# Kernel optimization log

Measured on AMD Instinct MI355X. Metric: run time of the kernel, lower is better.

## Reference

```python
import jax, jax.numpy as jnp
import numpy as np

HIDDEN = 16
PROJ = 2
INPUT = 2


def _gates_split(gates):
    # PyTorch LSTM gate order: input, forget, cell(g), output
    i, f, g, o = jnp.split(gates, 4, axis=-1)
    return jax.nn.sigmoid(i), jax.nn.sigmoid(f), jnp.tanh(g), jax.nn.sigmoid(o)


def setup_inputs() -> dict:
    key = jax.random.key(0)
    ks = jax.random.split(key, 7)
    B, T, nstep = 64, 8192, 4096
    bound = 1.0 / np.sqrt(HIDDEN)  # torch default LSTM init: U(-1/sqrt(H), 1/sqrt(H))
    u = lambda k, shp: jax.random.uniform(k, shp, jnp.float32, -bound, bound)
    return {
        "u_train": jax.random.normal(ks[0], (B, T, INPUT), jnp.float32),
        "y_train": jax.random.normal(ks[1], (B, T, INPUT), jnp.float32),
        "W_ih": u(ks[2], (4 * HIDDEN, INPUT)),   # weight_ih_l0
        "W_hh": u(ks[3], (4 * HIDDEN, PROJ)),    # weight_hh_l0 (proj_size -> input to gates)
        "b_ih": u(ks[4], (4 * HIDDEN,)),
        "b_hh": u(ks[5], (4 * HIDDEN,)),
        "W_hr": u(ks[6], (PROJ, HIDDEN)),        # projection weight_hr_l0
        "nstep": nstep,
    }


def reference(u_train, y_train, W_ih, W_hh, b_ih, b_hh, W_hr, nstep):
    b = b_ih + b_hh

    # --- estimate_state: each of the nstep single-step LSTM calls starts from
    # ZERO state (the original never threads state back in), so there is no
    # recurrence: vectorize over all nstep timesteps at once.
    x = y_train[:, :nstep, :]                       # [B, nstep, 2]
    gates = jnp.einsum("bti,gi->btg", x, W_ih) + b  # [B, nstep, 4H]; h-term is 0
    i, f, g, o = _gates_split(gates)
    c1 = i * g                                      # c0 = 0 => f*c0 vanishes
    y1 = jnp.einsum("bth,ph->btp", o * jnp.tanh(c1), W_hr)  # [B, nstep, PROJ]
    hn = y1[:, -1, :]                               # [B, PROJ]
    cn = c1[:, -1, :]                               # [B, HIDDEN]

    # --- predict_state: true recurrent LSTM with projection over the tail.
    def step(carry, x_t):
        h, c = carry                                # h:[B,PROJ] c:[B,HIDDEN]
        gt = x_t @ W_ih.T + h @ W_hh.T + b          # [B, 4H]
        i, f, g, o = _gates_split(gt)
        c = f * c + i * g
        h = (o * jnp.tanh(c)) @ W_hr.T              # [B, PROJ]
        return (h, c), h

    xs = jnp.swapaxes(u_train[:, nstep:, :], 0, 1)  # [T-nstep, B, 2]
    _, ys = jax.lax.scan(step, (hn, cn), xs)
    y2 = jnp.swapaxes(ys, 0, 1)                     # [B, T-nstep, PROJ]

    return jnp.concatenate([y1, y2], axis=1)        # [B, T, PROJ]
```

## Files before the change

kernel.cpp:

```cpp
#include <hip/hip_runtime.h>


#define BB   64
#define TT   8192
#define NST  4096
#define PF   16

static __device__ __forceinline__ float fast_exp2(float x) {
#if __has_builtin(__builtin_amdgcn_exp2f)
  return __builtin_amdgcn_exp2f(x);
#else
  return exp2f(x);
#endif
}
static __device__ __forceinline__ float fast_rcp(float x) {
#if __has_builtin(__builtin_amdgcn_rcpf)
  return __builtin_amdgcn_rcpf(x);
#else
  return 1.0f / x;
#endif
}

template <int CTRL>
static __device__ __forceinline__ float rr_add(float x) {
  int r = __builtin_amdgcn_update_dpp(0, __builtin_bit_cast(int, x), CTRL, 0xF, 0xF, true);
  return x + __builtin_bit_cast(float, r);
}

template <int SEL>
static __device__ __forceinline__ float qperm(float x) {
  int r = __builtin_amdgcn_update_dpp(0, __builtin_bit_cast(int, x), SEL, 0xF, 0xF, true);
  return __builtin_bit_cast(float, r);
}

static __device__ __forceinline__ float rdlane63(float x) {
  return __builtin_bit_cast(float,
      __builtin_amdgcn_readlane(__builtin_bit_cast(int, x), 63));
}

struct SW {
  float w0, w1, wh0, wh1, b;
  float m, n;
  float whr0, whr0m2, whr1, whr1m2;
};

static __device__ __forceinline__ void scan_step(const SW& w, float x0, float x1,
                                                 float& h0, float& h1, float& c) {
  const float bse = fmaf(w.w1, x1, fmaf(w.w0, x0, w.b));
  float s = fmaf(w.wh0, h0, bse);
  s = fmaf(w.wh1, h1, s);
  const float d = fast_rcp(1.f + fast_exp2(s));
  const float a = fmaf(d, w.m, w.n);
  const float gi = qperm<0x00>(a);
  const float gf = qperm<0x55>(a);
  const float gg = qperm<0xAA>(a);
  const float go = qperm<0xFF>(a);
  c = fmaf(gf, c, gi * gg);
  const float o0  = go * w.whr0;
  const float o0m = go * w.whr0m2;
  const float o1  = go * w.whr1;
  const float o1m = go * w.whr1m2;
  const float r2 = fast_rcp(1.f + fast_exp2(c * 2.8853900817779268f));
  float p0 = fmaf(r2, o0m, o0);
  float p1 = fmaf(r2, o1m, o1);
  p0 = rr_add<0x124>(p0); p1 = rr_add<0x124>(p1);
  p0 = rr_add<0x128>(p0); p1 = rr_add<0x128>(p1);
  p0 = rr_add<0x142>(p0); p1 = rr_add<0x142>(p1);
  p0 = rr_add<0x143>(p0); p1 = rr_add<0x143>(p1);
  h0 = rdlane63(p0);
  h1 = rdlane63(p1);
}

__global__ __launch_bounds__(256) void openlstm_kernel(
    const float* __restrict__ u_train, const float* __restrict__ y_train,
    const float* __restrict__ Wih, const float* __restrict__ Whh,
    const float* __restrict__ bih, const float* __restrict__ bhh,
    const float* __restrict__ Whr, float* __restrict__ out) {
  const int tid = threadIdx.x;
  const float S1 = -1.4426950408889634f;
  const float S2 = -2.8853900817779268f;

  if (blockIdx.x < 16) {
    const int lane = tid & 63;
    const int wv   = tid >> 6;
    const int bb   = blockIdx.x * 4 + wv;
    const int hh   = lane >> 2;
    const int r    = lane & 3;
    const int wrow = r * 16 + hh;
    const bool isg = (r == 2);
    const float sc = isg ? S2 : S1;

    SW w;
    w.w0  = Wih[2 * wrow] * sc;  w.w1  = Wih[2 * wrow + 1] * sc;
    w.wh0 = Whh[2 * wrow] * sc;  w.wh1 = Whh[2 * wrow + 1] * sc;
    w.b   = (bih[wrow] + bhh[wrow]) * sc;
    w.m   = isg ? 2.f : 1.f;
    w.n   = isg ? -1.f : 0.f;
    w.whr0   = Whr[hh];
    w.whr0m2 = -2.f * w.whr0;
    w.whr1   = Whr[16 + hh];
    w.whr1m2 = -2.f * w.whr1;

    float h0 = 0.f, h1 = 0.f, c = 0.f;
    {
      const float2 xv = *(const float2*)(y_train + ((size_t)bb * TT + (NST - 1)) * 2);
      scan_step(w, xv.x, xv.y, h0, h1, c);
    }

    const float* up = u_train + ((size_t)bb * TT + NST) * 2;
    float*       ob = out     + ((size_t)bb * TT + NST) * 2;

    float2 xb[PF];
#pragma unroll
    for (int k = 0; k < PF; ++k) xb[k] = *(const float2*)(up + 2 * k);

    const int  cslot = lane >> 1;
    const bool odd   = lane & 1;
    float cap = 0.f;

    for (int t = 0; t < NST; t += PF) {
#pragma unroll
      for (int k = 0; k < PF; ++k) {
        const float x0 = xb[k].x, x1 = xb[k].y;
        int tn = t + k + PF;
        tn = (tn < NST) ? tn : (NST - 1);
        xb[k] = *(const float2*)(up + (size_t)tn * 2);
        scan_step(w, x0, x1, h0, h1, c);
        const float hsel = odd ? h1 : h0;
        cap = (cslot == k) ? hsel : cap;
      }
      if (lane < 32) ob[(size_t)t * 2 + lane] = cap;
    }
  } else {
    const int hh  = tid & 15;
    const int grp = tid >> 4;
    const int gid = (blockIdx.x - 16) * 16 + grp;
    const int bb  = gid >> 12;
    const int t   = gid & (NST - 1);
    const int ri = hh, rg = hh + 32, ro = hh + 48;

    const float wii0 = Wih[2 * ri] * S1, wii1 = Wih[2 * ri + 1] * S1;
    const float wig0 = Wih[2 * rg] * S2, wig1 = Wih[2 * rg + 1] * S2;
    const float wio0 = Wih[2 * ro] * S1, wio1 = Wih[2 * ro + 1] * S1;
    const float bi = (bih[ri] + bhh[ri]) * S1;
    const float bg = (bih[rg] + bhh[rg]) * S2;
    const float bo = (bih[ro] + bhh[ro]) * S1;
    const float whr0 = Whr[hh], whr1 = Whr[16 + hh];

    const float2 xv = *(const float2*)(y_train + ((size_t)bb * TT + t) * 2);
    const float si = fmaf(wii1, xv.y, fmaf(wii0, xv.x, bi));
    const float sg = fmaf(wig1, xv.y, fmaf(wig0, xv.x, bg));
    const float so = fmaf(wio1, xv.y, fmaf(wio0, xv.x, bo));
    const float gi = fast_rcp(1.f + fast_exp2(si));
    const float gg = fmaf(2.f, fast_rcp(1.f + fast_exp2(sg)), -1.f);
    const float go = fast_rcp(1.f + fast_exp2(so));
    const float c1 = gi * gg;
    const float tc = fmaf(-2.f, fast_rcp(1.f + fast_exp2(c1 * 2.8853900817779268f)), 1.f);
    const float v  = go * tc;
    float p0 = v * whr0;
    float p1 = v * whr1;
    p0 = rr_add<0x128>(p0); p1 = rr_add<0x128>(p1);
    p0 = rr_add<0x124>(p0); p1 = rr_add<0x124>(p1);
    p0 = rr_add<0x122>(p0); p1 = rr_add<0x122>(p1);
    p0 = rr_add<0x121>(p0); p1 = rr_add<0x121>(p1);
    if (hh == 0) *(float2*)(out + ((size_t)bb * TT + t) * 2) = make_float2(p0, p1);
  }
}

extern "C" void kernel_launch(void* const* d_in, const int* in_sizes, int n_in,
                              void* d_out, int out_size, void* d_ws, size_t ws_size,
                              hipStream_t stream) {
  const float* u_train = (const float*)d_in[0];
  const float* y_train = (const float*)d_in[1];
  const float* Wih     = (const float*)d_in[2];
  const float* Whh     = (const float*)d_in[3];
  const float* bih     = (const float*)d_in[4];
  const float* bhh     = (const float*)d_in[5];
  const float* Whr     = (const float*)d_in[6];
  float* out = (float*)d_out;

  const int grid = 16 + (BB * NST) / 16;
  openlstm_kernel<<<grid, 256, 0, stream>>>(u_train, y_train, Wih, Whh, bih,
                                            bhh, Whr, out);
}
```

Before: 457.8 us.

## Prescale cell state, raise scan wave priority, simplify input prefetch and output stores

The recurrent cell state is now kept prescaled by 2*log2(e), with the g-gate affine constants adjusted to match, so one multiply drops off the serial critical path each step. The scan waves call s_setprio(1) so they get scheduling priority over the co-resident parallel-phase waves. The 16-deep register prefetch ring and lane-captured 32-wide stores are replaced by a one-step-ahead float4 load covering two timesteps and a per-pair float4 store from every lane. The shallower prefetch could expose load latency on the serial chain, and having every lane store each pair adds redundant memory traffic.

```diff
diff --git a/kernel.cpp b/kernel.cpp
--- a/kernel.cpp
+++ b/kernel.cpp
@@ -4,7 +4,6 @@
 #define BB   64
 #define TT   8192
 #define NST  4096
-#define PF   16
 
 static __device__ __forceinline__ float fast_exp2(float x) {
 #if __has_builtin(__builtin_amdgcn_exp2f)
@@ -45,7 +44,7 @@
 };
 
 static __device__ __forceinline__ void scan_step(const SW& w, float x0, float x1,
-                                                 float& h0, float& h1, float& c) {
+                                                 float& h0, float& h1, float& C) {
   const float bse = fmaf(w.w1, x1, fmaf(w.w0, x0, w.b));
   float s = fmaf(w.wh0, h0, bse);
   s = fmaf(w.wh1, h1, s);
@@ -55,12 +54,12 @@
   const float gf = qperm<0x55>(a);
   const float gg = qperm<0xAA>(a);
   const float go = qperm<0xFF>(a);
-  c = fmaf(gf, c, gi * gg);
+  C = fmaf(gf, C, gi * gg);
   const float o0  = go * w.whr0;
   const float o0m = go * w.whr0m2;
   const float o1  = go * w.whr1;
   const float o1m = go * w.whr1m2;
-  const float r2 = fast_rcp(1.f + fast_exp2(c * 2.8853900817779268f));
+  const float r2 = fast_rcp(1.f + fast_exp2(C));
   float p0 = fmaf(r2, o0m, o0);
   float p1 = fmaf(r2, o1m, o1);
   p0 = rr_add<0x124>(p0); p1 = rr_add<0x124>(p1);
@@ -81,6 +80,7 @@
   const float S2 = -2.8853900817779268f;
 
   if (blockIdx.x < 16) {
+    __builtin_amdgcn_s_setprio(1);
     const int lane = tid & 63;
     const int wv   = tid >> 6;
     const int bb   = blockIdx.x * 4 + wv;
@@ -94,42 +94,37 @@
     w.w0  = Wih[2 * wrow] * sc;  w.w1  = Wih[2 * wrow + 1] * sc;
     w.wh0 = Whh[2 * wrow] * sc;  w.wh1 = Whh[2 * wrow + 1] * sc;
     w.b   = (bih[wrow] + bhh[wrow]) * sc;
-    w.m   = isg ? 2.f : 1.f;
-    w.n   = isg ? -1.f : 0.f;
+    w.m   = isg ? 5.7707801635558536f : 1.f;
+    w.n   = isg ? -2.8853900817779268f : 0.f;
     w.whr0   = Whr[hh];
     w.whr0m2 = -2.f * w.whr0;
     w.whr1   = Whr[16 + hh];
     w.whr1m2 = -2.f * w.whr1;
 
-    float h0 = 0.f, h1 = 0.f, c = 0.f;
+    float h0 = 0.f, h1 = 0.f, C = 0.f;
     {
       const float2 xv = *(const float2*)(y_train + ((size_t)bb * TT + (NST - 1)) * 2);
-      scan_step(w, xv.x, xv.y, h0, h1, c);
+      scan_step(w, xv.x, xv.y, h0, h1, C);
     }
 
     const float* up = u_train + ((size_t)bb * TT + NST) * 2;
-    float*       ob = out     + ((size_t)bb * TT + NST) * 2;
+    float*       op = out     + ((size_t)bb * TT + NST) * 2;
 
-    float2 xb[PF];
-#pragma unroll
-    for (int k = 0; k < PF; ++k) xb[k] = *(const float2*)(up + 2 * k);
-
-    const int  cslot = lane >> 1;
-    const bool odd   = lane & 1;
-    float cap = 0.f;
-
-    for (int t = 0; t < NST; t += PF) {
-#pragma unroll
-      for (int k = 0; k < PF; ++k) {
-        const float x0 = xb[k].x, x1 = xb[k].y;
-        int tn = t + k + PF;
-        tn = (tn < NST) ? tn : (NST - 1);
-        xb[k] = *(const float2*)(up + (size_t)tn * 2);
-        scan_step(w, x0, x1, h0, h1, c);
-        const float hsel = odd ? h1 : h0;
-        cap = (cslot == k) ? hsel : cap;
-      }
-      if (lane < 32) ob[(size_t)t * 2 + lane] = cap;
+    float4 xq = *(const float4*)(up);
+#pragma unroll 4
+    for (int p = 0; p < NST / 2 - 1; ++p) {
+      const float4 xn = *(const float4*)(up + (size_t)(p + 1) * 4);
+      scan_step(w, xq.x, xq.y, h0, h1, C);
+      const float ha0 = h0, ha1 = h1;
+      scan_step(w, xq.z, xq.w, h0, h1, C);
+      *(float4*)(op + (size_t)p * 4) = make_float4(ha0, ha1, h0, h1);
+      xq = xn;
+    }
+    {
+      scan_step(w, xq.x, xq.y, h0, h1, C);
+      const float ha0 = h0, ha1 = h1;
+      scan_step(w, xq.z, xq.w, h0, h1, C);
+      *(float4*)(op + (size_t)(NST / 2 - 1) * 4) = make_float4(ha0, ha1, h0, h1);
     }
   } else {
     const int hh  = tid & 15;
```

Measured after the change: 499.0 us. 1.09x slower.
